# Kernel optimization log

Hardware: AMD Instinct MI355X
Metric: run time of the kernel (lower is better)

The kernel has to match this reference:

```python
import jax, jax.numpy as jnp
import numpy as np

MAX_WORDS = 128  # static word capacity (stands in for dynamic max_word_num)


def setup_inputs() -> dict:
    key = jax.random.key(0)
    k1, k2 = jax.random.split(key)
    L, B, D = 512, 256, 256
    char_feats = jax.random.normal(k1, (L, B, D), dtype=jnp.float32)
    # sorted random word ids, densified so each row's ids are contiguous 0..n-1
    raw = jnp.sort(jax.random.randint(k2, (B, L), 0, MAX_WORDS), axis=1)
    bump = jnp.concatenate(
        [jnp.zeros((B, 1), jnp.int32), (raw[:, 1:] != raw[:, :-1]).astype(jnp.int32)],
        axis=1,
    )
    word_ids = jnp.cumsum(bump, axis=1)  # [B, L], non-decreasing, < MAX_WORDS
    attention_mask = jnp.ones((B, L), dtype=jnp.int32)
    return {"char_feats": char_feats, "word_ids": word_ids, "attention_mask": attention_mask}


def _pool(char_feats, word_ids, attention_mask):
    # char_feats: [L, B, D] time-major; word_ids/attention_mask: [B, L]
    L, B, D = char_feats.shape
    char_nums = jnp.sum(attention_mask, axis=1) - 2  # drop [CLS]/[SEP]
    pos = jnp.arange(L)
    # chars at positions 1 .. char_nums (inclusive) participate, per torch slicing
    valid = (pos[None, :] >= 1) & (pos[None, :] < 1 + char_nums[:, None])  # [B, L]
    seg = jnp.where(valid, word_ids, MAX_WORDS)  # overflow bucket for invalid chars
    feats_bld = jnp.transpose(char_feats, (1, 0, 2))  # [B, L, D]

    seg_sum = jax.vmap(
        lambda s, f: jax.ops.segment_sum(f, s, num_segments=MAX_WORDS + 1)
    )(seg, feats_bld)[:, :MAX_WORDS]  # [B, W, D]
    counts = jax.vmap(
        lambda s: jax.ops.segment_sum(jnp.ones((L,), jnp.float32), s, num_segments=MAX_WORDS + 1)
    )(seg)[:, :MAX_WORDS]  # [B, W]

    word_nums = jnp.max(word_ids, axis=1) + 1  # [B]
    masks = jnp.arange(MAX_WORDS)[:, None] < word_nums[None, :]  # [W, B]
    means = seg_sum / jnp.maximum(counts, 1.0)[..., None]  # counts>=1 within word_num
    word_feats = jnp.where(masks.T[..., None], means, 0.0)  # zero padded word slots
    return jnp.transpose(word_feats, (1, 0, 2)), masks  # [W, B, D], [W, B]


def reference(char_feats, word_ids, attention_mask):
    return _pool(char_feats, word_ids, attention_mask)
```

## Files before the change

kernel.cpp:

```cpp
#include <hip/hip_runtime.h>
#include <hip/hip_bf16.h>

#define LSEQ 512
#define BATCH 256
#define DIM 256
#define WMAX 128
#define ROW4 (BATCH * DIM / 4)
#define BD4 (DIM / 4)
#define MSTRIDE (WMAX + 2)

__global__ __launch_bounds__(256) void meta_kernel(
    const int* __restrict__ word_ids,
    const int* __restrict__ amask,
    int* __restrict__ meta,
    float* __restrict__ out)
{
    const int b = blockIdx.x;
    const int t = threadIdx.x;
    const int lane = t & 63;
    const int wi = t >> 6;

    __shared__ int sids[LSEQ];
    __shared__ int spart[4];
    __shared__ int sstart[WMAX + 1];

    int msum = 0;
    if (t < 128) {
        ((int4*)sids)[t] = ((const int4*)(word_ids + b * LSEQ))[t];
    } else {
        int4 m = ((const int4*)(amask + b * LSEQ))[t - 128];
        msum = m.x + m.y + m.z + m.w;
    }
    #pragma unroll
    for (int off = 32; off; off >>= 1) msum += __shfl_down(msum, off, 64);
    if (lane == 0) spart[wi] = msum;
    __syncthreads();

    const int char_num = spart[0] + spart[1] + spart[2] + spart[3] - 2;
    int pend = 1 + char_num;
    if (pend < 1) pend = 1;
    if (pend > LSEQ) pend = LSEQ;

    if (t <= WMAX) sstart[t] = pend;
    __syncthreads();

    for (int p = 1 + t; p < pend; p += 256) {
        if (p == 1 || sids[p] != sids[p - 1]) sstart[sids[p]] = p;
    }
    if (t == 0) sstart[0] = 1;
    __syncthreads();

    if (t <= WMAX) meta[b * MSTRIDE + t] = sstart[t];

    if (t < WMAX) {
        int word_num = sids[LSEQ - 1] + 1;
        out[(size_t)WMAX * BATCH * DIM + (size_t)t * BATCH + b] =
            (t < word_num) ? 1.0f : 0.0f;
    }
}

__global__ __launch_bounds__(256) void pool_kernel(
    const float* __restrict__ feats,
    const int* __restrict__ meta,
    float* __restrict__ out)
{
    const int b = blockIdx.x & (BATCH - 1);
    const int wg = blockIdx.x >> 8;
    const int t = threadIdx.x;
    const int lane = t & 63;
    const int w = wg * 4 + (t >> 6);

    const int* m = meta + b * MSTRIDE;
    const int s0 = m[w];
    const int s1 = m[w + 1];
    const int c = s1 - s0;

    const float4* __restrict__ f4 = (const float4*)feats;
    const int boff = b * BD4 + lane;

    float4 acc = make_float4(0.f, 0.f, 0.f, 0.f);
    for (int i = 0; i < c; i += 8) {
        const int n = c - i;
        float4 v[8];
        #pragma unroll
        for (int j = 0; j < 8; j++) {
            if (j < n) v[j] = f4[(size_t)(s0 + i + j) * ROW4 + boff];
        }
        #pragma unroll
        for (int j = 0; j < 8; j++) {
            if (j < n) {
                acc.x += v[j].x; acc.y += v[j].y;
                acc.z += v[j].z; acc.w += v[j].w;
            }
        }
    }

    const float inv = 1.0f / (float)(c > 0 ? c : 1);
    ((float4*)out)[(size_t)w * ROW4 + boff] =
        make_float4(acc.x * inv, acc.y * inv, acc.z * inv, acc.w * inv);
}

extern "C" void kernel_launch(void* const* d_in, const int* in_sizes, int n_in,
                              void* d_out, int out_size, void* d_ws, size_t ws_size,
                              hipStream_t stream) {
    const float* char_feats = (const float*)d_in[0];
    const int* word_ids     = (const int*)d_in[1];
    const int* amask        = (const int*)d_in[2];
    float* out              = (float*)d_out;
    int* meta               = (int*)d_ws;

    meta_kernel<<<BATCH, 256, 0, stream>>>(word_ids, amask, meta, out);
    pool_kernel<<<BATCH * 32, 256, 0, stream>>>(char_feats, meta, out);
}
```

Baseline: 203.4 us.

## Fuse segment-boundary computation into pooling kernel, removing metadata pass

Merges the metadata kernel into the pooling kernel. Each block now reloads word_ids and the attention mask for its batch row and finds start positions only for its own four words in shared memory. This removes one kernel launch and the global workspace round trip. In exchange, the small 4KB id and mask loads and the boundary scan are repeated across 32 blocks per batch row.

```diff
diff --git a/kernel.cpp b/kernel.cpp
--- a/kernel.cpp
+++ b/kernel.cpp
@@ -1,5 +1,4 @@
 #include <hip/hip_runtime.h>
-#include <hip/hip_bf16.h>
 
 #define LSEQ 512
 #define BATCH 256
@@ -7,22 +6,24 @@
 #define WMAX 128
 #define ROW4 (BATCH * DIM / 4)
 #define BD4 (DIM / 4)
-#define MSTRIDE (WMAX + 2)
+#define WPB 4
 
-__global__ __launch_bounds__(256) void meta_kernel(
+__global__ __launch_bounds__(256) void fused_pool_kernel(
+    const float* __restrict__ feats,
     const int* __restrict__ word_ids,
     const int* __restrict__ amask,
-    int* __restrict__ meta,
     float* __restrict__ out)
 {
-    const int b = blockIdx.x;
-    const int t = threadIdx.x;
+    const int b    = blockIdx.x & (BATCH - 1);
+    const int wg   = blockIdx.x >> 8;
+    const int t    = threadIdx.x;
     const int lane = t & 63;
-    const int wi = t >> 6;
+    const int wi   = t >> 6;
+    const int w0   = wg * WPB;
 
     __shared__ int sids[LSEQ];
     __shared__ int spart[4];
-    __shared__ int sstart[WMAX + 1];
+    __shared__ int sstart[WPB + 1];
 
     int msum = 0;
     if (t < 128) {
@@ -41,42 +42,30 @@
     if (pend < 1) pend = 1;
     if (pend > LSEQ) pend = LSEQ;
 
-    if (t <= WMAX) sstart[t] = pend;
+    if (t <= WPB) sstart[t] = pend;
     __syncthreads();
 
     for (int p = 1 + t; p < pend; p += 256) {
-        if (p == 1 || sids[p] != sids[p - 1]) sstart[sids[p]] = p;
+        const int id = sids[p];
+        if ((p == 1 || id != sids[p - 1]) && id >= w0 && id <= w0 + WPB)
+            sstart[id - w0] = p;
     }
-    if (t == 0) sstart[0] = 1;
+    if (t == 0 && wg == 0) sstart[0] = 1;
     __syncthreads();
 
-    if (t <= WMAX) meta[b * MSTRIDE + t] = sstart[t];
-
-    if (t < WMAX) {
-        int word_num = sids[LSEQ - 1] + 1;
+    if (wg == 0 && t < WMAX) {
+        const int word_num = sids[LSEQ - 1] + 1;
         out[(size_t)WMAX * BATCH * DIM + (size_t)t * BATCH + b] =
             (t < word_num) ? 1.0f : 0.0f;
     }
-}
 
-__global__ __launch_bounds__(256) void pool_kernel(
-    const float* __restrict__ feats,
-    const int* __restrict__ meta,
-    float* __restrict__ out)
-{
-    const int b = blockIdx.x & (BATCH - 1);
-    const int wg = blockIdx.x >> 8;
-    const int t = threadIdx.x;
-    const int lane = t & 63;
-    const int w = wg * 4 + (t >> 6);
-
-    const int* m = meta + b * MSTRIDE;
-    const int s0 = m[w];
-    const int s1 = m[w + 1];
-    const int c = s1 - s0;
+    const int s0 = sstart[wi];
+    const int s1 = sstart[wi + 1];
+    const int c  = s1 - s0;
 
     const float4* __restrict__ f4 = (const float4*)feats;
     const int boff = b * BD4 + lane;
+    const int w = w0 + wi;
 
     float4 acc = make_float4(0.f, 0.f, 0.f, 0.f);
     for (int i = 0; i < c; i += 8) {
@@ -107,8 +96,8 @@
     const int* word_ids     = (const int*)d_in[1];
     const int* amask        = (const int*)d_in[2];
     float* out              = (float*)d_out;
-    int* meta               = (int*)d_ws;
+    (void)d_ws; (void)ws_size;
 
-    meta_kernel<<<BATCH, 256, 0, stream>>>(word_ids, amask, meta, out);
-    pool_kernel<<<BATCH * 32, 256, 0, stream>>>(char_feats, meta, out);
+    fused_pool_kernel<<<(WMAX / WPB) * BATCH, 256, 0, stream>>>(
+        char_feats, word_ids, amask, out);
 }
```

New measurement: 201.9 us. No clear change (-0.8%).
